# Kernel tuning notes

Measured on AMD Instinct MI355X. Metric: run time of the kernel, lower is better.

## Reference

```python
import jax, jax.numpy as jnp
import numpy as np

HIDDEN = 300
DEPTH = 3
MAX_NB = 10
AFEAT = 82
BFEAT = 6
B, N, M = 16, 2048, 4096


def setup_inputs() -> dict:
    key = jax.random.key(0)
    ks = jax.random.split(key, 16)
    s = 0.05
    return {
        "input_atom": jax.random.normal(ks[0], (B, N, AFEAT), jnp.float32),
        "input_bond": jax.random.normal(ks[1], (B, M, BFEAT), jnp.float32),
        "node_mask": jnp.ones((B, N, 1), jnp.float32),
        "atom_graph": jax.random.randint(ks[2], (B, N, MAX_NB), 0, N, jnp.int32),
        "bond_graph": jax.random.randint(ks[3], (B, N, MAX_NB), 0, M, jnp.int32),
        "num_nbs": jax.random.randint(ks[4], (B, N), 0, MAX_NB, jnp.int32),
        "W_af": jax.random.normal(ks[5], (AFEAT, HIDDEN), jnp.float32) * s,
        "W_na": jax.random.normal(ks[6], (HIDDEN, HIDDEN), jnp.float32) * s,
        "W_nb": jax.random.normal(ks[7], (BFEAT, HIDDEN), jnp.float32) * s,
        "W_sa": jax.random.normal(ks[8], (HIDDEN, HIDDEN), jnp.float32) * s,
        "W_u2": jax.random.normal(ks[9], (HIDDEN + BFEAT, HIDDEN), jnp.float32) * s,
        "b_u2": jnp.zeros((HIDDEN,), jnp.float32),
        "W_u1": jax.random.normal(ks[10], (2 * HIDDEN, HIDDEN), jnp.float32) * s,
        "b_u1": jnp.zeros((HIDDEN,), jnp.float32),
        "W_out": jax.random.normal(ks[11], (HIDDEN, 1), jnp.float32) * s,
        "b_out": jnp.zeros((1,), jnp.float32),
    }


def _wln(input_atom, input_bond, node_mask, atom_graph, bond_graph, num_nbs,
         W_af, W_na, W_nb, W_sa, W_u2, b_u2, W_u1, b_u1):
    bidx = jnp.arange(input_atom.shape[0])[:, None, None]  # (B,1,1)
    atom_feat = jax.nn.relu(input_atom @ W_af)             # (B,N,H)
    fbond_nei = input_bond[bidx, bond_graph]               # (B,N,max_nb,6) gather
    h_nei_bond = fbond_nei @ W_nb                          # constant over depth
    # neighbor validity mask from num_nbs (sequence mask)
    nb_mask = (jnp.arange(MAX_NB)[None, None, :] < num_nbs[..., None]
               ).astype(atom_feat.dtype)[..., None]        # (B,N,max_nb,1)
    kernel = None
    for _ in range(DEPTH):
        fatom_nei = atom_feat[bidx, atom_graph]            # (B,N,max_nb,H) gather
        h_nei = (fatom_nei @ W_na) * h_nei_bond
        f_nei = jnp.sum(h_nei * nb_mask, axis=-2)          # (B,N,H)
        f_self = atom_feat @ W_sa
        kernel = f_nei * f_self * node_mask                # last-layer WLN kernel
        l_nei = jnp.concatenate([fatom_nei, fbond_nei], axis=-1)
        pre_label = jax.nn.relu(l_nei @ W_u2 + b_u2)
        nei_label = jnp.sum(pre_label * nb_mask, axis=-2)
        new_label = jnp.concatenate([atom_feat, nei_label], axis=-1)
        atom_feat = jax.nn.relu(new_label @ W_u1 + b_u1)
    return kernel


def reference(input_atom, input_bond, node_mask, atom_graph, bond_graph, num_nbs,
              W_af, W_na, W_nb, W_sa, W_u2, b_u2, W_u1, b_u1, W_out, b_out):
    x = _wln(input_atom, input_bond, node_mask, atom_graph, bond_graph, num_nbs,
             W_af, W_na, W_nb, W_sa, W_u2, b_u2, W_u1, b_u1)  # (B,N,H)
    x = jnp.sum(x, axis=-2)                                   # sum pooling -> (B,H)
    return x @ W_out + b_out                                  # (B,1)
```

## Files before the change

kernel.cpp:

```cpp
#include <hip/hip_runtime.h>
#include <math.h>


typedef unsigned short ushort_t;
typedef __attribute__((ext_vector_type(8))) short bf16x8;
typedef __attribute__((ext_vector_type(8))) unsigned short ushort8;
typedef __attribute__((ext_vector_type(4))) float f32x4;

static constexpr int Hh  = 300;
static constexpr int Hp  = 320;
static constexpr int Bn  = 16;
static constexpr int Nn  = 2048;
static constexpr int Rn  = Bn * Nn;
static constexpr int NBn = 10;

static constexpr size_t OFF_U2 = 320 * 96;
static constexpr size_t OFF_NA = OFF_U2 + 320 * 320;
static constexpr size_t OFF_SA = OFF_NA + 320 * 320;
static constexpr size_t OFF_U1 = OFF_SA + 320 * 320;
static constexpr int    W_ELEMS = (int)(OFF_U1 + 320 * 640);

__device__ __forceinline__ ushort_t f2bf(float x) {
    union { float f; unsigned u; } c; c.f = x;
    unsigned r = c.u + 0x7FFFu + ((c.u >> 16) & 1u);
    return (ushort_t)(r >> 16);
}
__device__ __forceinline__ float bf2f(ushort_t h) {
    union { float f; unsigned u; } c; c.u = ((unsigned)h) << 16;
    return c.f;
}

__device__ __forceinline__ void stage16(const void* g, void* l) {
#if __has_builtin(__builtin_amdgcn_global_load_lds)
    __builtin_amdgcn_global_load_lds(
        (const __attribute__((address_space(1))) void*)g,
        (__attribute__((address_space(3))) void*)l, 16, 0, 0);
#else
    *(ushort8*)l = *(const ushort8*)g;
#endif
}

__device__ __forceinline__ float rfl_f(float v) {
    return __int_as_float(__builtin_amdgcn_readfirstlane(__float_as_int(v)));
}

template<bool RELU, bool BIAS, bool CONCAT>
__global__ __launch_bounds__(256)
void mfma_gemm_k(const ushort_t* __restrict__ A, const ushort_t* __restrict__ A2,
                 int lda, int KP,
                 const ushort_t* __restrict__ Wt,
                 const float* __restrict__ bias,
                 ushort_t* __restrict__ C)
{
    __shared__ __attribute__((aligned(16))) ushort_t As[128 * 32];
    __shared__ __attribute__((aligned(16))) ushort_t Bs[64 * 32];

    const int t    = threadIdx.x;
    const int wv   = t >> 6;
    const int ln   = t & 63;
    const int lrow = ln & 15;
    const int lgrp = ln >> 4;
    const int rowBase = blockIdx.y * 128;
    const int nBase   = blockIdx.x * 64;

    f32x4 acc[2][4];
#pragma unroll
    for (int i = 0; i < 2; i++)
#pragma unroll
        for (int j = 0; j < 4; j++) acc[i][j] = (f32x4){0.f, 0.f, 0.f, 0.f};

    const int half = KP >> 1;

    for (int k0 = 0; k0 < KP; k0 += 32) {
#pragma unroll
        for (int e = 0; e < 2; e++) {
            int chunk = t + e * 256;
            int r = chunk >> 2, c = chunk & 3;
            int k = k0 + c * 8;
            const ushort_t* src;
            if (CONCAT && k >= half) src = A2 + (size_t)(rowBase + r) * lda + (k - half);
            else                     src = A  + (size_t)(rowBase + r) * lda + k;
            stage16(src, &As[(size_t)chunk * 8]);
        }
        {
            int r = t >> 2, c = t & 3;
            stage16(Wt + (size_t)(nBase + r) * KP + k0 + c * 8, &Bs[(size_t)t * 8]);
        }
        __syncthreads();

        bf16x8 af[2], bfr[4];
#pragma unroll
        for (int mb = 0; mb < 2; mb++)
            af[mb] = *(const bf16x8*)&As[(wv * 32 + mb * 16 + lrow) * 32 + lgrp * 8];
#pragma unroll
        for (int nb = 0; nb < 4; nb++)
            bfr[nb] = *(const bf16x8*)&Bs[(nb * 16 + lrow) * 32 + lgrp * 8];
#pragma unroll
        for (int mb = 0; mb < 2; mb++)
#pragma unroll
            for (int nb = 0; nb < 4; nb++)
                acc[mb][nb] = __builtin_amdgcn_mfma_f32_16x16x32_bf16(
                    af[mb], bfr[nb], acc[mb][nb], 0, 0, 0);
        __syncthreads();
    }

#pragma unroll
    for (int mb = 0; mb < 2; mb++) {
        int row0 = rowBase + wv * 32 + mb * 16 + lgrp * 4;
#pragma unroll
        for (int nb = 0; nb < 4; nb++) {
            int col = nBase + nb * 16 + lrow;
            float bv = 0.f;
            if (BIAS) bv = (col < Hh) ? bias[col] : 0.f;
#pragma unroll
            for (int r = 0; r < 4; r++) {
                float v = acc[mb][nb][r] + bv;
                if (RELU) v = v > 0.f ? v : 0.f;
                C[(size_t)(row0 + r) * Hp + col] = f2bf(v);
            }
        }
    }
}

template<bool FINAL>
__global__ __launch_bounds__(256)
void gather_k(const ushort_t* __restrict__ Arow,
              const ushort_t* __restrict__ Asa,
              const float* __restrict__ bond,
              const float* __restrict__ Wb,
              const float* __restrict__ bias,
              const int*   __restrict__ ag,
              const int*   __restrict__ bg,
              const int*   __restrict__ nnb,
              const float* __restrict__ nmask,
              const float* __restrict__ Wout,
              void* __restrict__ outp)
{
    __shared__ float sWb[6 * Hp];
    __shared__ float sV[Hp];
    __shared__ __attribute__((aligned(16))) ushort_t sAtom[4][NBn][Hp];
    __shared__ float sdot[4];
    for (int i = threadIdx.x; i < 6 * Hp; i += 256) {
        int tt = i / Hp, h = i - tt * Hp;
        sWb[i] = (h < Hh) ? Wb[tt * Hh + h] : 0.f;
    }
    for (int i = threadIdx.x; i < Hp; i += 256) {
        float v = 0.f;
        if (i < Hh) v = FINAL ? Wout[i] : bias[i];
        sV[i] = v;
    }
    __syncthreads();

    const int wave = threadIdx.x >> 6;
    const int lane = threadIdx.x & 63;
    const int node = blockIdx.x * 4 + wave;
    const int b    = node >> 11;
    const int nn   = nnb[node];
    const int base = node * NBn;
    const size_t arow0 = (size_t)(b << 11) * Hp;
    const size_t brow0 = (size_t)(b << 12) * 6;

    const int iav = ag[base + (lane < 10 ? lane : 9)];
    const int ibv = bg[base + (lane < 10 ? lane : 9)];

    float tmpc[NBn][6];
#pragma unroll
    for (int k = 0; k < NBn; k++) {
        if (k < nn) {
            int ibk = __shfl(ibv, k);
            const float* pf = bond + brow0 + (size_t)ibk * 6;
#pragma unroll
            for (int tt = 0; tt < 6; tt++) tmpc[k][tt] = pf[tt];
        }
    }
#pragma unroll
    for (int k = 0; k < NBn; k++) {
        if (k < nn) {
            int iak = __shfl(iav, k);
            const ushort_t* pa = Arow + arow0 + (size_t)iak * Hp;
            if (lane < 40)
                stage16(pa + (size_t)lane * 8, &sAtom[wave][k][lane * 8]);
        }
    }
    float c[NBn][6];
#pragma unroll
    for (int k = 0; k < NBn; k++) {
        if (k < nn) {
#pragma unroll
            for (int tt = 0; tt < 6; tt++) c[k][tt] = rfl_f(tmpc[k][tt]);
        }
    }
    asm volatile("s_waitcnt vmcnt(0)" ::: "memory");

    float acc[5];
#pragma unroll
    for (int j = 0; j < 5; j++) {
        const int h = lane + j * 64;
        const float w0 = sWb[h],          w1 = sWb[Hp + h],     w2 = sWb[2 * Hp + h];
        const float w3 = sWb[3 * Hp + h], w4 = sWb[4 * Hp + h], w5 = sWb[5 * Hp + h];
        const float sv = FINAL ? 0.f : sV[h];
        float a = 0.f;
#pragma unroll
        for (int k = 0; k < NBn; k++) {
            if (k < nn) {
                float av = bf2f(sAtom[wave][k][h]);
                float w  = c[k][0] * w0 + c[k][1] * w1 + c[k][2] * w2
                         + c[k][3] * w3 + c[k][4] * w4 + c[k][5] * w5;
                if (FINAL) {
                    a += av * w;
                } else {
                    float v = av + w + sv;
                    a += v > 0.f ? v : 0.f;
                }
            }
        }
        acc[j] = a;
    }

    if (FINAL) {
        const ushort_t* psa = Asa + (size_t)node * Hp + lane;
        float dot = 0.f;
#pragma unroll
        for (int j = 0; j < 5; j++) {
            int h = lane + j * 64;
            dot += acc[j] * bf2f(psa[j * 64]) * sV[h];
        }
        dot *= nmask[node];
#pragma unroll
        for (int off = 32; off > 0; off >>= 1) dot += __shfl_down(dot, off, 64);
        if (lane == 0) sdot[wave] = dot;
        __syncthreads();
        if (threadIdx.x == 0)
            atomicAdd(&((float*)outp)[b], sdot[0] + sdot[1] + sdot[2] + sdot[3]);
    } else {
        ushort_t* pl = (ushort_t*)outp + (size_t)node * Hp + lane;
#pragma unroll
        for (int j = 0; j < 5; j++) {
            int h = lane + j * 64;
            pl[j * 64] = (h < Hh) ? f2bf(acc[j]) : (ushort_t)0;
        }
    }
}

__global__ void zero_k(ushort_t* __restrict__ p, int n)
{
    int i = blockIdx.x * 256 + threadIdx.x;
    if (i < n) p[i] = 0;
}

__global__ void cvt_atom_k(const float* __restrict__ src, ushort_t* __restrict__ dst)
{
    int idx = blockIdx.x * 256 + threadIdx.x;
    if (idx >= Rn * 96) return;
    int r = idx / 96, c = idx - r * 96;
    dst[idx] = (c < 82) ? f2bf(src[r * 82 + c]) : (ushort_t)0;
}

__global__ void cvt_weights_k(const float* __restrict__ W_af,
                              const float* __restrict__ W_u2,
                              const float* __restrict__ W_na,
                              const float* __restrict__ W_sa,
                              const float* __restrict__ W_u1,
                              ushort_t* __restrict__ dst0)
{
    const float* src; int Ksrc, kbase, stride; size_t doff;
    switch (blockIdx.y) {
    case 0:  src = W_af;             Ksrc =  82; kbase = 0;   stride =  96; doff = 0;      break;
    case 1:  src = W_u2;             Ksrc = 300; kbase = 0;   stride = 320; doff = OFF_U2; break;
    case 2:  src = W_na;             Ksrc = 300; kbase = 0;   stride = 320; doff = OFF_NA; break;
    case 3:  src = W_sa;             Ksrc = 300; kbase = 0;   stride = 320; doff = OFF_SA; break;
    case 4:  src = W_u1;             Ksrc = 300; kbase = 0;   stride = 640; doff = OFF_U1; break;
    default: src = W_u1 + 300 * 300; Ksrc = 300; kbase = 320; stride = 640; doff = OFF_U1; break;
    }
    int idx = blockIdx.x * 256 + threadIdx.x;
    if (idx >= Ksrc * Hh) return;
    int k = idx / Hh, n = idx - k * Hh;
    dst0[doff + (size_t)n * stride + kbase + k] = f2bf(src[idx]);
}

__global__ void init_out_k(float* __restrict__ out, const float* __restrict__ b_out)
{
    if (threadIdx.x < Bn) out[threadIdx.x] = b_out[0];
}

extern "C" void kernel_launch(void* const* d_in, const int* in_sizes, int n_in,
                              void* d_out, int out_size, void* d_ws, size_t ws_size,
                              hipStream_t stream)
{
    const float* input_atom = (const float*)d_in[0];
    const float* input_bond = (const float*)d_in[1];
    const float* node_mask  = (const float*)d_in[2];
    const int*   atom_graph = (const int*)d_in[3];
    const int*   bond_graph = (const int*)d_in[4];
    const int*   num_nbs    = (const int*)d_in[5];
    const float* W_af       = (const float*)d_in[6];
    const float* W_na       = (const float*)d_in[7];
    const float* W_nb       = (const float*)d_in[8];
    const float* W_sa       = (const float*)d_in[9];
    const float* W_u2       = (const float*)d_in[10];
    const float* b_u2       = (const float*)d_in[11];
    const float* W_u1       = (const float*)d_in[12];
    const float* b_u1       = (const float*)d_in[13];
    const float* W_out      = (const float*)d_in[14];
    const float* b_out      = (const float*)d_in[15];
    float* out = (float*)d_out;

    const float* W_u2b = W_u2 + (size_t)Hh * Hh;

    const size_t S2 = (size_t)Rn * Hp;
    ushort_t* bufA0 = (ushort_t*)d_ws;
    ushort_t* bufA1 = bufA0 + S2;
    ushort_t* bufP  = bufA1 + S2;
    ushort_t* bufL  = bufP  + S2;
    ushort_t* bufS  = bufL  + S2;
    ushort_t* iaB   = bufS  + S2;
    ushort_t* wAf   = iaB + (size_t)Rn * 96;

    zero_k<<<(W_ELEMS + 255) / 256, 256, 0, stream>>>(wAf, W_ELEMS);
    cvt_atom_k<<<(Rn * 96 + 255) / 256, 256, 0, stream>>>(input_atom, iaB);
    cvt_weights_k<<<dim3(352, 6), 256, 0, stream>>>(W_af, W_u2, W_na, W_sa, W_u1, wAf);
    init_out_k<<<dim3(1), dim3(64), 0, stream>>>(out, b_out);

    dim3 gg(5, Rn / 128);
    const int gb = Rn / 4;

    mfma_gemm_k<true, false, false><<<gg, 256, 0, stream>>>(
        iaB, nullptr, 96, 96, wAf, nullptr, bufA0);

    ushort_t* cur = bufA0;
    ushort_t* oth = bufA1;
    for (int d = 0; d < 2; d++) {
        mfma_gemm_k<false, false, false><<<gg, 256, 0, stream>>>(
            cur, nullptr, Hp, Hp, wAf + OFF_U2, nullptr, bufP);
        gather_k<false><<<gb, 256, 0, stream>>>(
            bufP, nullptr, input_bond, W_u2b, b_u2,
            atom_graph, bond_graph, num_nbs, nullptr, nullptr, bufL);
        mfma_gemm_k<true, true, true><<<gg, 256, 0, stream>>>(
            cur, bufL, Hp, 2 * Hp, wAf + OFF_U1, b_u1, oth);
        ushort_t* tmp = cur; cur = oth; oth = tmp;
    }

    mfma_gemm_k<false, false, false><<<gg, 256, 0, stream>>>(
        cur, nullptr, Hp, Hp, wAf + OFF_NA, nullptr, bufP);
    mfma_gemm_k<false, false, false><<<gg, 256, 0, stream>>>(
        cur, nullptr, Hp, Hp, wAf + OFF_SA, nullptr, bufS);
    gather_k<true><<<gb, 256, 0, stream>>>(
        bufP, bufS, input_bond, W_nb, nullptr,
        atom_graph, bond_graph, num_nbs, node_mask, W_out, out);
}
```

Measured before the change: 576.1 us.

## Enlarge GEMM tiles, remap blocks per XCD by batch, pad LDS

The GEMM tile grows from 128x64 to 256x64 rows per block, so each wave computes a 64x64 sub-tile. LDS rows are padded to 40 elements to reduce bank conflicts, and loads go through registers instead of direct global-to-LDS staging. Both the GEMM and gather kernels remap block IDs so that each XCD handles whole batches, which improves L2 locality for the random neighbor gathers. The gather output is now written with nontemporal stores. The trade-off is more registers and LDS per block, fewer GEMM blocks (640), and the loss of the asynchronous LDS load path.

```diff
diff --git a/kernel.cpp b/kernel.cpp
--- a/kernel.cpp
+++ b/kernel.cpp
@@ -31,13 +31,9 @@
 }
 
 __device__ __forceinline__ void stage16(const void* g, void* l) {
-#if __has_builtin(__builtin_amdgcn_global_load_lds)
     __builtin_amdgcn_global_load_lds(
         (const __attribute__((address_space(1))) void*)g,
         (__attribute__((address_space(3))) void*)l, 16, 0, 0);
-#else
-    *(ushort8*)l = *(const ushort8*)g;
-#endif
 }
 
 __device__ __forceinline__ float rfl_f(float v) {
@@ -52,20 +48,27 @@
                  const float* __restrict__ bias,
                  ushort_t* __restrict__ C)
 {
-    __shared__ __attribute__((aligned(16))) ushort_t As[128 * 32];
-    __shared__ __attribute__((aligned(16))) ushort_t Bs[64 * 32];
-
-    const int t    = threadIdx.x;
-    const int wv   = t >> 6;
-    const int ln   = t & 63;
+    __shared__ __attribute__((aligned(16))) ushort_t As[256 * 40];
+    __shared__ __attribute__((aligned(16))) ushort_t Bs[64 * 40];
+
+    const int id   = blockIdx.x;
+    const int xcd  = id & 7;
+    const int slot = id >> 3;
+    const int bsel = slot / 40;
+    const int sub  = slot % 40;
+    const int batch = xcd + 8 * bsel;
+    const int rowBase = (batch * 8 + sub / 5) * 256;
+    const int nBase   = (sub % 5) * 64;
+
+    const int t   = threadIdx.x;
+    const int wv  = t >> 6;
+    const int ln  = t & 63;
     const int lrow = ln & 15;
     const int lgrp = ln >> 4;
-    const int rowBase = blockIdx.y * 128;
-    const int nBase   = blockIdx.x * 64;
-
-    f32x4 acc[2][4];
-#pragma unroll
-    for (int i = 0; i < 2; i++)
+
+    f32x4 acc[4][4];
+#pragma unroll
+    for (int i = 0; i < 4; i++)
 #pragma unroll
         for (int j = 0; j < 4; j++) acc[i][j] = (f32x4){0.f, 0.f, 0.f, 0.f};
 
@@ -73,30 +76,31 @@
 
     for (int k0 = 0; k0 < KP; k0 += 32) {
 #pragma unroll
-        for (int e = 0; e < 2; e++) {
+        for (int e = 0; e < 4; e++) {
             int chunk = t + e * 256;
             int r = chunk >> 2, c = chunk & 3;
             int k = k0 + c * 8;
             const ushort_t* src;
             if (CONCAT && k >= half) src = A2 + (size_t)(rowBase + r) * lda + (k - half);
             else                     src = A  + (size_t)(rowBase + r) * lda + k;
-            stage16(src, &As[(size_t)chunk * 8]);
+            *(ushort8*)&As[r * 40 + c * 8] = *(const ushort8*)src;
         }
         {
             int r = t >> 2, c = t & 3;
-            stage16(Wt + (size_t)(nBase + r) * KP + k0 + c * 8, &Bs[(size_t)t * 8]);
+            *(ushort8*)&Bs[r * 40 + c * 8] =
+                *(const ushort8*)(Wt + (size_t)(nBase + r) * KP + k0 + c * 8);
         }
         __syncthreads();
 
-        bf16x8 af[2], bfr[4];
-#pragma unroll
-        for (int mb = 0; mb < 2; mb++)
-            af[mb] = *(const bf16x8*)&As[(wv * 32 + mb * 16 + lrow) * 32 + lgrp * 8];
+        bf16x8 af[4], bfr[4];
+#pragma unroll
+        for (int mb = 0; mb < 4; mb++)
+            af[mb] = *(const bf16x8*)&As[(wv * 64 + mb * 16 + lrow) * 40 + lgrp * 8];
 #pragma unroll
         for (int nb = 0; nb < 4; nb++)
-            bfr[nb] = *(const bf16x8*)&Bs[(nb * 16 + lrow) * 32 + lgrp * 8];
-#pragma unroll
-        for (int mb = 0; mb < 2; mb++)
+            bfr[nb] = *(const bf16x8*)&Bs[(nb * 16 + lrow) * 40 + lgrp * 8];
+#pragma unroll
+        for (int mb = 0; mb < 4; mb++)
 #pragma unroll
             for (int nb = 0; nb < 4; nb++)
                 acc[mb][nb] = __builtin_amdgcn_mfma_f32_16x16x32_bf16(
@@ -105,8 +109,8 @@
     }
 
 #pragma unroll
-    for (int mb = 0; mb < 2; mb++) {
-        int row0 = rowBase + wv * 32 + mb * 16 + lgrp * 4;
+    for (int mb = 0; mb < 4; mb++) {
+        int row0 = rowBase + wv * 64 + mb * 16 + lgrp * 4;
 #pragma unroll
         for (int nb = 0; nb < 4; nb++) {
             int col = nBase + nb * 16 + lrow;
@@ -153,8 +157,14 @@
 
     const int wave = threadIdx.x >> 6;
     const int lane = threadIdx.x & 63;
-    const int node = blockIdx.x * 4 + wave;
-    const int b    = node >> 11;
+
+    const int id  = blockIdx.x;
+    const int xcd = id & 7;
+    const int r_  = id >> 3;
+    const int b   = xcd + 8 * (r_ & 1);
+    const int grp = r_ >> 1;
+    const int node = b * Nn + grp * 4 + wave;
+
     const int nn   = nnb[node];
     const int base = node * NBn;
     const size_t arow0 = (size_t)(b << 11) * Hp;
@@ -237,7 +247,8 @@
 #pragma unroll
         for (int j = 0; j < 5; j++) {
             int h = lane + j * 64;
-            pl[j * 64] = (h < Hh) ? f2bf(acc[j]) : (ushort_t)0;
+            ushort_t v = (h < Hh) ? f2bf(acc[j]) : (ushort_t)0;
+            __builtin_nontemporal_store(v, pl + j * 64);
         }
     }
 }
@@ -321,28 +332,28 @@
     cvt_weights_k<<<dim3(352, 6), 256, 0, stream>>>(W_af, W_u2, W_na, W_sa, W_u1, wAf);
     init_out_k<<<dim3(1), dim3(64), 0, stream>>>(out, b_out);
 
-    dim3 gg(5, Rn / 128);
+    const int gemmBlocks = 640;
     const int gb = Rn / 4;
 
-    mfma_gemm_k<true, false, false><<<gg, 256, 0, stream>>>(
+    mfma_gemm_k<true, false, false><<<gemmBlocks, 256, 0, stream>>>(
         iaB, nullptr, 96, 96, wAf, nullptr, bufA0);
 
     ushort_t* cur = bufA0;
     ushort_t* oth = bufA1;
     for (int d = 0; d < 2; d++) {
-        mfma_gemm_k<false, false, false><<<gg, 256, 0, stream>>>(
+        mfma_gemm_k<false, false, false><<<gemmBlocks, 256, 0, stream>>>(
             cur, nullptr, Hp, Hp, wAf + OFF_U2, nullptr, bufP);
         gather_k<false><<<gb, 256, 0, stream>>>(
             bufP, nullptr, input_bond, W_u2b, b_u2,
             atom_graph, bond_graph, num_nbs, nullptr, nullptr, bufL);
-        mfma_gemm_k<true, true, true><<<gg, 256, 0, stream>>>(
+        mfma_gemm_k<true, true, true><<<gemmBlocks, 256, 0, stream>>>(
             cur, bufL, Hp, 2 * Hp, wAf + OFF_U1, b_u1, oth);
         ushort_t* tmp = cur; cur = oth; oth = tmp;
     }
 
-    mfma_gemm_k<false, false, false><<<gg, 256, 0, stream>>>(
+    mfma_gemm_k<false, false, false><<<gemmBlocks, 256, 0, stream>>>(
         cur, nullptr, Hp, Hp, wAf + OFF_NA, nullptr, bufP);
-    mfma_gemm_k<false, false, false><<<gg, 256, 0, stream>>>(
+    mfma_gemm_k<false, false, false><<<gemmBlocks, 256, 0, stream>>>(
         cur, nullptr, Hp, Hp, wAf + OFF_SA, nullptr, bufS);
     gather_k<true><<<gb, 256, 0, stream>>>(
         bufP, bufS, input_bond, W_nb, nullptr,
```

Result: faster. 504.8 us (-12.4%).
